# Optimization experiments

Measured on AMD Instinct MI355X. Metric: run time of the kernel, lower is better.

## Reference

```python
import jax, jax.numpy as jnp
import numpy as np
from jax import lax

BN_EPS = 1e-5

def _dw_conv_bn(img, w, g, b, mu, var):
    # img: [B,C,H,W], w: [C,1,3,3] depthwise (feature_group_count=C), stride 1, pad 1
    C = img.shape[1]
    y = lax.conv_general_dilated(img, w, (1, 1), 'SAME',
                                 dimension_numbers=('NCHW', 'OIHW', 'NCHW'),
                                 feature_group_count=C)
    scale = (g / jnp.sqrt(var + BN_EPS))[None, :, None, None]
    return y * scale + (b - mu * g / jnp.sqrt(var + BN_EPS))[None, :, None, None]


def setup_inputs() -> dict:
    key = jax.random.key(0)
    B, H, W, C, Co = 32, 28, 28, 192, 192
    T = 1 + H * W
    ks = jax.random.split(key, 8)
    x = jax.random.normal(ks[0], (B, T, C), dtype=jnp.float32)
    conv_w = jax.random.normal(ks[1], (3, C, 1, 3, 3), dtype=jnp.float32) * 0.1
    bn_scale = 1.0 + 0.1 * jax.random.normal(ks[2], (3, C), dtype=jnp.float32)
    bn_bias = 0.1 * jax.random.normal(ks[3], (3, C), dtype=jnp.float32)
    bn_mean = 0.1 * jax.random.normal(ks[4], (3, C), dtype=jnp.float32)
    bn_var = jax.random.uniform(ks[5], (3, C), dtype=jnp.float32, minval=0.5, maxval=1.5)
    w_qkv = jax.random.normal(ks[6], (3, Co, C), dtype=jnp.float32) / np.sqrt(C)
    kp, kb = jax.random.split(ks[7])
    w_proj = jax.random.normal(kp, (Co, Co), dtype=jnp.float32) / np.sqrt(Co)
    b_proj = 0.01 * jax.random.normal(kb, (Co,), dtype=jnp.float32)
    return {"x": x, "conv_w": conv_w, "bn_scale": bn_scale, "bn_bias": bn_bias,
            "bn_mean": bn_mean, "bn_var": bn_var, "w_qkv": w_qkv,
            "w_proj": w_proj, "b_proj": b_proj, "h": H, "w": W, "num_heads": 3}


def reference(x, conv_w, bn_scale, bn_bias, bn_mean, bn_var, w_qkv, w_proj, b_proj, h, w, num_heads):
    B, T, C = x.shape
    Co = w_proj.shape[0]
    scale = Co ** (-0.5)  # NOTE: module scales by dim_out^-0.5, not per-head
    cls_tok, tok = x[:, :1], x[:, 1:]
    img = tok.reshape(B, h, w, C).transpose(0, 3, 1, 2)  # b (h w) c -> b c h w
    qkv = []
    for i in range(3):  # q, k, v conv projections (depthwise conv + BN inference)
        y = _dw_conv_bn(img, conv_w[i], bn_scale[i], bn_bias[i], bn_mean[i], bn_var[i])
        y = y.reshape(B, C, h * w).transpose(0, 2, 1)  # b c h w -> b (h w) c
        y = jnp.concatenate([cls_tok, y], axis=1)      # prepend cls token
        qkv.append(jnp.einsum('btc,oc->bto', y, w_qkv[i]))
    d = Co // num_heads
    q, k, v = (t.reshape(B, T, num_heads, d).transpose(0, 2, 1, 3) for t in qkv)
    attn = jnp.einsum('bhld,bhtd->bhlt', q, k) * scale
    attn = jax.nn.softmax(attn, axis=-1)
    out = jnp.einsum('bhlt,bhtd->bhld', attn, v)
    out = out.transpose(0, 2, 1, 3).reshape(B, T, Co)
    return out @ w_proj.T + b_proj
```

## Files before the change

### kernel.cpp

```cpp
#include <hip/hip_runtime.h>

#define B_   32
#define Hh   28
#define Ww   28
#define Cc   192
#define T_   785
#define BT_  (B_ * T_)
#define BTC_ ((size_t)BT_ * Cc)
#define SCALE2 0.10412163388f

typedef __attribute__((ext_vector_type(8))) __bf16 bf16x8;
typedef __attribute__((ext_vector_type(4))) __bf16 bf16x4;
typedef __attribute__((ext_vector_type(4))) float  f32x4;

__global__ __launch_bounds__(192) void conv3_bn_k(
    const float* __restrict__ x, const float* __restrict__ cw,
    const float* __restrict__ g, const float* __restrict__ bb,
    const float* __restrict__ mu, const float* __restrict__ var,
    __bf16* __restrict__ y,
    const float* __restrict__ wqkv, const float* __restrict__ wproj,
    __bf16* __restrict__ wdst)
{
  const int c = threadIdx.x;
  const int h = blockIdx.x;
  const int b = blockIdx.y;
  if (h == Hh) {
    int t = b * 192 + c;
    int base = t * 24;
    const float* src = (base < 3 * Cc * Cc) ? (wqkv + base)
                                            : (wproj + (base - 3 * Cc * Cc));
#pragma unroll
    for (int e = 0; e < 24; e += 4) {
      float4 v = *(const float4*)(src + e);
      wdst[base + e + 0] = (__bf16)v.x;
      wdst[base + e + 1] = (__bf16)v.y;
      wdst[base + e + 2] = (__bf16)v.z;
      wdst[base + e + 3] = (__bf16)v.w;
    }
    return;
  }
  float w9[3][9], sc[3], sh[3];
#pragma unroll
  for (int br = 0; br < 3; ++br) {
    sc[br] = g[br * Cc + c] * rsqrtf(var[br * Cc + c] + 1e-5f);
    sh[br] = bb[br * Cc + c] - mu[br * Cc + c] * sc[br];
#pragma unroll
    for (int k = 0; k < 9; ++k) w9[br][k] = cw[(br * Cc + c) * 9 + k];
  }
  const float* xb = x + (size_t)b * T_ * Cc;
  if (h == 0) {
#pragma unroll
    for (int br = 0; br < 3; ++br)
      y[br * BTC_ + (size_t)b * T_ * Cc + c] = (__bf16)xb[c];
  }
  float c0[3], c1[3], c2[3];
#pragma unroll
  for (int r = 0; r < 3; ++r) {
    int rr = h - 1 + r;
    c0[r] = 0.f;
    c1[r] = (rr >= 0 && rr < Hh) ? xb[(size_t)(1 + rr * Ww) * Cc + c] : 0.f;
  }
  for (int col = 0; col < Ww; ++col) {
#pragma unroll
    for (int r = 0; r < 3; ++r) {
      int rr = h - 1 + r, ci = col + 1;
      c2[r] = (rr >= 0 && rr < Hh && ci < Ww)
                ? xb[(size_t)(1 + rr * Ww + ci) * Cc + c] : 0.f;
    }
    size_t orow = (size_t)(b * T_ + 1 + h * Ww + col) * Cc + c;
#pragma unroll
    for (int br = 0; br < 3; ++br) {
      float acc = c0[0]*w9[br][0] + c1[0]*w9[br][1] + c2[0]*w9[br][2]
                + c0[1]*w9[br][3] + c1[1]*w9[br][4] + c2[1]*w9[br][5]
                + c0[2]*w9[br][6] + c1[2]*w9[br][7] + c2[2]*w9[br][8];
      y[br * BTC_ + orow] = (__bf16)(acc * sc[br] + sh[br]);
    }
#pragma unroll
    for (int r = 0; r < 3; ++r) { c0[r] = c1[r]; c1[r] = c2[r]; }
  }
}

template <int MODE>
__global__ __launch_bounds__(512) void gemm_bf16(
    const __bf16* __restrict__ A0, const __bf16* __restrict__ W0,
    const float* __restrict__ bias, void* __restrict__ outp)
{
  __shared__ __bf16 As[128][72];
  __shared__ __bf16 Bs[192][72];
  const int z = blockIdx.z;
  const __bf16* A  = A0 + (MODE == 0 ? (size_t)z * BTC_ : 0);
  const __bf16* Bw = W0 + (MODE == 0 ? (size_t)z * Cc * Cc : 0);
  const float osc = (MODE == 0 && z == 0) ? SCALE2 : 1.0f;
  const int tid = threadIdx.x;
  const int wid = tid >> 6, l = tid & 63, c = l & 15, g = l >> 4;
  const int wm = wid >> 2, wn = wid & 3;
  const int m0 = blockIdx.x * 128;
  const int ar = tid >> 2, aq = tid & 3;
  const int brow = tid >> 3, bv = tid & 7;

  f32x4 acc[4][3];
#pragma unroll
  for (int i = 0; i < 4; ++i)
#pragma unroll
    for (int j = 0; j < 3; ++j) acc[i][j] = (f32x4)(0.f);

  const __bf16* ap = A + (size_t)(m0 + ar) * Cc + aq * 16;
  const __bf16* bp0 = Bw + (size_t)brow * Cc + bv * 8;
  uint4 a0 = *(const uint4*)(ap + 0);
  uint4 a1 = *(const uint4*)(ap + 8);
  uint4 b0 = *(const uint4*)(bp0 + 0 * 64 * Cc / 1);
  uint4 b1 = *(const uint4*)(bp0 + (size_t)64 * Cc);
  uint4 b2 = *(const uint4*)(bp0 + (size_t)128 * Cc);

  for (int kc = 0; kc < 3; ++kc) {
    __syncthreads();
    *(uint4*)&As[ar][aq * 16 + 0] = a0;
    *(uint4*)&As[ar][aq * 16 + 8] = a1;
    *(uint4*)&Bs[brow +   0][bv * 8] = b0;
    *(uint4*)&Bs[brow +  64][bv * 8] = b1;
    *(uint4*)&Bs[brow + 128][bv * 8] = b2;
    if (kc < 2) {
      ap += 64; bp0 += 64;
      a0 = *(const uint4*)(ap + 0);
      a1 = *(const uint4*)(ap + 8);
      b0 = *(const uint4*)(bp0);
      b1 = *(const uint4*)(bp0 + (size_t)64 * Cc);
      b2 = *(const uint4*)(bp0 + (size_t)128 * Cc);
    }
    __syncthreads();
#pragma unroll
    for (int ksl = 0; ksl < 2; ++ksl) {
      bf16x8 af[4], bfr[3];
#pragma unroll
      for (int mf = 0; mf < 4; ++mf)
        af[mf] = *(const bf16x8*)&As[wm * 64 + mf * 16 + c][ksl * 32 + g * 8];
#pragma unroll
      for (int nf = 0; nf < 3; ++nf)
        bfr[nf] = *(const bf16x8*)&Bs[wn * 48 + nf * 16 + c][ksl * 32 + g * 8];
      __builtin_amdgcn_s_setprio(1);
#pragma unroll
      for (int mf = 0; mf < 4; ++mf)
#pragma unroll
        for (int nf = 0; nf < 3; ++nf)
          acc[mf][nf] = __builtin_amdgcn_mfma_f32_16x16x32_bf16(
              af[mf], bfr[nf], acc[mf][nf], 0, 0, 0);
      __builtin_amdgcn_s_setprio(0);
    }
  }
  float bias_c[3] = {0.f, 0.f, 0.f};
  if (MODE == 1) {
#pragma unroll
    for (int nf = 0; nf < 3; ++nf) bias_c[nf] = bias[wn * 48 + nf * 16 + c];
  }
#pragma unroll
  for (int mf = 0; mf < 4; ++mf) {
#pragma unroll
    for (int i = 0; i < 4; ++i) {
      int m = m0 + wm * 64 + mf * 16 + g * 4 + i;
      if (m < BT_) {
#pragma unroll
        for (int nf = 0; nf < 3; ++nf) {
          int n = wn * 48 + nf * 16 + c;
          if (MODE == 1)
            ((float*)outp)[(size_t)m * Cc + n] = acc[mf][nf][i] + bias_c[nf];
          else
            ((__bf16*)outp)[z * BTC_ + (size_t)m * Cc + n] =
                (__bf16)(acc[mf][nf][i] * osc);
        }
      }
    }
  }
}

__global__ __launch_bounds__(256) void attn_mfma(
    const __bf16* __restrict__ qkv, __bf16* __restrict__ aout)
{
  __shared__ __bf16 Ks[64][72];
  __shared__ __bf16 Vt[64][72];
  __shared__ __bf16 Ps[4][16][72];
  const int bid = blockIdx.x;
  const int swz = (bid & 7) * 84 + (bid >> 3);
  const int qt = swz % 7;
  const int g2 = swz / 7;
  const int hh = g2 % 3;
  const int b  = g2 / 3;
  const int tid = threadIdx.x;
  const int wid = tid >> 6, l = tid & 63, c = l & 15, g = l >> 4;
  const __bf16* Q = qkv + ((size_t)(0 * B_ + b) * T_) * Cc + hh * 64;
  const __bf16* K = qkv + ((size_t)(1 * B_ + b) * T_) * Cc + hh * 64;
  const __bf16* V = qkv + ((size_t)(2 * B_ + b) * T_) * Cc + hh * 64;

  const int q0 = qt * 128 + wid * 32;
  bf16x8 qf[2][2];
#pragma unroll
  for (int s = 0; s < 2; ++s) {
    const __bf16* qp = Q + (size_t)(q0 + s * 16 + c) * Cc + g * 8;
    qf[s][0] = *(const bf16x8*)(qp);
    qf[s][1] = *(const bf16x8*)(qp + 32);
  }

  const int skey = tid >> 2, sdq = tid & 3;
  const int vkp = tid & 31, vd0 = (tid >> 5) * 8;
  const __bf16* kp  = K + (size_t)skey * Cc + sdq * 16;
  const __bf16* vp0 = V + (size_t)(2 * vkp + 0) * Cc + vd0;
  const __bf16* vp1 = V + (size_t)(2 * vkp + 1) * Cc + vd0;
  uint4 kr0 = *(const uint4*)(kp + 0);
  uint4 kr1 = *(const uint4*)(kp + 8);
  uint4 va  = *(const uint4*)vp0;
  uint4 vb  = *(const uint4*)vp1;

  f32x4 ot[2][4];
#pragma unroll
  for (int s = 0; s < 2; ++s)
#pragma unroll
    for (int f = 0; f < 4; ++f) ot[s][f] = (f32x4)(0.f);
  float m_run[2] = {-1e30f, -1e30f};
  float l_run[2] = {0.f, 0.f};

  for (int kt = 0; kt < 13; ++kt) {
    __syncthreads();
    *(uint4*)&Ks[skey][sdq * 16 + 0] = kr0;
    *(uint4*)&Ks[skey][sdq * 16 + 8] = kr1;
    {
      const ushort* pa = (const ushort*)&va;
      const ushort* pb = (const ushort*)&vb;
#pragma unroll
      for (int e = 0; e < 8; ++e) {
        unsigned pk2 = (unsigned)pa[e] | ((unsigned)pb[e] << 16);
        *(unsigned*)&Vt[vd0 + e][2 * vkp] = pk2;
      }
    }
    if (kt < 12) {
      kp += 64 * Cc; vp0 += 64 * Cc; vp1 += 64 * Cc;
      kr0 = *(const uint4*)(kp + 0);
      kr1 = *(const uint4*)(kp + 8);
      va  = *(const uint4*)vp0;
      vb  = *(const uint4*)vp1;
    }
    __syncthreads();

#pragma unroll
    for (int set = 0; set < 2; ++set) {
      f32x4 st[4];
#pragma unroll
      for (int f = 0; f < 4; ++f) st[f] = (f32x4)(0.f);
      __builtin_amdgcn_s_setprio(1);
#pragma unroll
      for (int s2 = 0; s2 < 2; ++s2) {
#pragma unroll
        for (int f = 0; f < 4; ++f) {
          bf16x8 ka = *(const bf16x8*)&Ks[f * 16 + c][s2 * 32 + g * 8];
          st[f] = __builtin_amdgcn_mfma_f32_16x16x32_bf16(ka, qf[set][s2], st[f], 0, 0, 0);
        }
      }
      __builtin_amdgcn_s_setprio(0);
      if (kt == 12) {
#pragma unroll
        for (int f = 0; f < 4; ++f)
#pragma unroll
          for (int i = 0; i < 4; ++i)
            if (f * 16 + g * 4 + i >= 17) st[f][i] = -1e30f;
      }
      float pmax = -1e30f;
#pragma unroll
      for (int f = 0; f < 4; ++f)
#pragma unroll
        for (int i = 0; i < 4; ++i) pmax = fmaxf(pmax, st[f][i]);
      pmax = fmaxf(pmax, __shfl_xor(pmax, 16));
      pmax = fmaxf(pmax, __shfl_xor(pmax, 32));
      if (!__all(pmax <= m_run[set] + 8.f)) {
        float mnew = fmaxf(m_run[set], pmax);
        float corr = exp2f(m_run[set] - mnew);
        m_run[set] = mnew;
        l_run[set] *= corr;
#pragma unroll
        for (int f = 0; f < 4; ++f)
#pragma unroll
          for (int i = 0; i < 4; ++i) ot[set][f][i] *= corr;
      }
      float rs = 0.f;
#pragma unroll
      for (int f = 0; f < 4; ++f) {
        bf16x4 pk;
#pragma unroll
        for (int i = 0; i < 4; ++i) {
          float p = exp2f(st[f][i] - m_run[set]);
          rs += p;
          pk[i] = (__bf16)p;
        }
        *(bf16x4*)&Ps[wid][c][f * 16 + g * 4] = pk;
      }
      rs += __shfl_xor(rs, 16);
      rs += __shfl_xor(rs, 32);
      l_run[set] += rs;

      __builtin_amdgcn_s_setprio(1);
#pragma unroll
      for (int s2 = 0; s2 < 2; ++s2) {
        bf16x8 pb2 = *(const bf16x8*)&Ps[wid][c][s2 * 32 + g * 8];
#pragma unroll
        for (int f = 0; f < 4; ++f) {
          bf16x8 va2 = *(const bf16x8*)&Vt[f * 16 + c][s2 * 32 + g * 8];
          ot[set][f] = __builtin_amdgcn_mfma_f32_16x16x32_bf16(va2, pb2, ot[set][f], 0, 0, 0);
        }
      }
      __builtin_amdgcn_s_setprio(0);
    }
  }

#pragma unroll
  for (int set = 0; set < 2; ++set) {
    const int t = q0 + set * 16 + c;
    if (t < T_) {
      float inv = 1.f / l_run[set];
      __bf16* op = aout + ((size_t)(b * T_ + t)) * Cc + hh * 64;
#pragma unroll
      for (int f = 0; f < 4; ++f) {
        bf16x4 ov;
#pragma unroll
        for (int i = 0; i < 4; ++i) ov[i] = (__bf16)(ot[set][f][i] * inv);
        *(bf16x4*)(op + f * 16 + g * 4) = ov;
      }
    }
  }
}

extern "C" void kernel_launch(void* const* d_in, const int* in_sizes, int n_in,
                              void* d_out, int out_size, void* d_ws, size_t ws_size,
                              hipStream_t stream) {
  (void)in_sizes; (void)n_in; (void)out_size; (void)ws_size;
  const float* x        = (const float*)d_in[0];
  const float* conv_w   = (const float*)d_in[1];
  const float* bn_scale = (const float*)d_in[2];
  const float* bn_bias  = (const float*)d_in[3];
  const float* bn_mean  = (const float*)d_in[4];
  const float* bn_var   = (const float*)d_in[5];
  const float* w_qkv    = (const float*)d_in[6];
  const float* w_proj   = (const float*)d_in[7];
  const float* b_proj   = (const float*)d_in[8];

  __bf16* ybf  = (__bf16*)d_ws;
  __bf16* qkvb = ybf + 3 * BTC_;
  __bf16* aobf = qkvb + 3 * BTC_;
  __bf16* wq   = aobf + BTC_;
  __bf16* wp   = wq + 3 * Cc * Cc;

  conv3_bn_k<<<dim3(Hh + 1, B_), 192, 0, stream>>>(
      x, conv_w, bn_scale, bn_bias, bn_mean, bn_var, ybf, w_qkv, w_proj, wq);

  const int mblocks = (BT_ + 127) / 128;
  gemm_bf16<0><<<dim3(mblocks, 1, 3), 512, 0, stream>>>(ybf, wq, nullptr, qkvb);
  attn_mfma<<<672, 256, 0, stream>>>(qkvb, aobf);
  gemm_bf16<1><<<dim3(mblocks, 1, 1), 512, 0, stream>>>(aobf, wp, b_proj, d_out);
}
```

Measured before the change: 179.4 us.

## Double-buffer attention K/V tiles, halve query tile, and block conv over rows

The attention kernel now double-buffers K and V in LDS with one barrier per key tile. It also halves the query rows per block from 128 to 64, which raises the grid from 672 to 1248 blocks, and the swizzle is updated to match. The conv kernel now has each block compute 4 output rows, so neighbouring input rows are reused across row outputs and the grid shrinks from 29x32 to 8x32 blocks. The intent is more overlap and occupancy in attention and fewer redundant input loads in conv, at the cost of reloading K/V once per smaller query tile and fewer, longer conv blocks.

Measured after the change: 177.0 us. No clear change (-1.3%).

```diff
diff --git a/kernel.cpp b/kernel.cpp
--- a/kernel.cpp
+++ b/kernel.cpp
@@ -22,9 +22,9 @@
     __bf16* __restrict__ wdst)
 {
   const int c = threadIdx.x;
-  const int h = blockIdx.x;
+  const int bx = blockIdx.x;
   const int b = blockIdx.y;
-  if (h == Hh) {
+  if (bx == 7) {
     int t = b * 192 + c;
     int base = t * 24;
     const float* src = (base < 3 * Cc * Cc) ? (wqkv + base)
@@ -39,6 +39,7 @@
     }
     return;
   }
+  const int h0 = bx * 4;
   float w9[3][9], sc[3], sh[3];
 #pragma unroll
   for (int br = 0; br < 3; ++br) {
@@ -48,35 +49,38 @@
     for (int k = 0; k < 9; ++k) w9[br][k] = cw[(br * Cc + c) * 9 + k];
   }
   const float* xb = x + (size_t)b * T_ * Cc;
-  if (h == 0) {
+  if (bx == 0) {
 #pragma unroll
     for (int br = 0; br < 3; ++br)
       y[br * BTC_ + (size_t)b * T_ * Cc + c] = (__bf16)xb[c];
   }
-  float c0[3], c1[3], c2[3];
-#pragma unroll
-  for (int r = 0; r < 3; ++r) {
-    int rr = h - 1 + r;
+  float c0[6], c1[6], c2[6];
+#pragma unroll
+  for (int r = 0; r < 6; ++r) {
+    int rr = h0 - 1 + r;
     c0[r] = 0.f;
     c1[r] = (rr >= 0 && rr < Hh) ? xb[(size_t)(1 + rr * Ww) * Cc + c] : 0.f;
   }
   for (int col = 0; col < Ww; ++col) {
 #pragma unroll
-    for (int r = 0; r < 3; ++r) {
-      int rr = h - 1 + r, ci = col + 1;
+    for (int r = 0; r < 6; ++r) {
+      int rr = h0 - 1 + r, ci = col + 1;
       c2[r] = (rr >= 0 && rr < Hh && ci < Ww)
                 ? xb[(size_t)(1 + rr * Ww + ci) * Cc + c] : 0.f;
     }
-    size_t orow = (size_t)(b * T_ + 1 + h * Ww + col) * Cc + c;
-#pragma unroll
-    for (int br = 0; br < 3; ++br) {
-      float acc = c0[0]*w9[br][0] + c1[0]*w9[br][1] + c2[0]*w9[br][2]
-                + c0[1]*w9[br][3] + c1[1]*w9[br][4] + c2[1]*w9[br][5]
-                + c0[2]*w9[br][6] + c1[2]*w9[br][7] + c2[2]*w9[br][8];
-      y[br * BTC_ + orow] = (__bf16)(acc * sc[br] + sh[br]);
-    }
-#pragma unroll
-    for (int r = 0; r < 3; ++r) { c0[r] = c1[r]; c1[r] = c2[r]; }
+#pragma unroll
+    for (int ro = 0; ro < 4; ++ro) {
+      size_t orow = (size_t)(b * T_ + 1 + (h0 + ro) * Ww + col) * Cc + c;
+#pragma unroll
+      for (int br = 0; br < 3; ++br) {
+        float acc = c0[ro+0]*w9[br][0] + c1[ro+0]*w9[br][1] + c2[ro+0]*w9[br][2]
+                  + c0[ro+1]*w9[br][3] + c1[ro+1]*w9[br][4] + c2[ro+1]*w9[br][5]
+                  + c0[ro+2]*w9[br][6] + c1[ro+2]*w9[br][7] + c2[ro+2]*w9[br][8];
+        y[br * BTC_ + orow] = (__bf16)(acc * sc[br] + sh[br]);
+      }
+    }
+#pragma unroll
+    for (int r = 0; r < 6; ++r) { c0[r] = c1[r]; c1[r] = c2[r]; }
   }
 }
 
@@ -108,7 +112,7 @@
   const __bf16* bp0 = Bw + (size_t)brow * Cc + bv * 8;
   uint4 a0 = *(const uint4*)(ap + 0);
   uint4 a1 = *(const uint4*)(ap + 8);
-  uint4 b0 = *(const uint4*)(bp0 + 0 * 64 * Cc / 1);
+  uint4 b0 = *(const uint4*)(bp0);
   uint4 b1 = *(const uint4*)(bp0 + (size_t)64 * Cc);
   uint4 b2 = *(const uint4*)(bp0 + (size_t)128 * Cc);
 
@@ -175,13 +179,13 @@
 __global__ __launch_bounds__(256) void attn_mfma(
     const __bf16* __restrict__ qkv, __bf16* __restrict__ aout)
 {
-  __shared__ __bf16 Ks[64][72];
-  __shared__ __bf16 Vt[64][72];
+  __shared__ __bf16 Ks[2][64][72];
+  __shared__ __bf16 Vt[2][64][72];
   __shared__ __bf16 Ps[4][16][72];
   const int bid = blockIdx.x;
-  const int swz = (bid & 7) * 84 + (bid >> 3);
-  const int qt = swz % 7;
-  const int g2 = swz / 7;
+  const int swz = (bid & 7) * 156 + (bid >> 3);
+  const int qt = swz % 13;
+  const int g2 = swz / 13;
   const int hh = g2 % 3;
   const int b  = g2 / 3;
   const int tid = threadIdx.x;
@@ -190,137 +194,134 @@
   const __bf16* K = qkv + ((size_t)(1 * B_ + b) * T_) * Cc + hh * 64;
   const __bf16* V = qkv + ((size_t)(2 * B_ + b) * T_) * Cc + hh * 64;
 
-  const int q0 = qt * 128 + wid * 32;
-  bf16x8 qf[2][2];
-#pragma unroll
-  for (int s = 0; s < 2; ++s) {
-    const __bf16* qp = Q + (size_t)(q0 + s * 16 + c) * Cc + g * 8;
-    qf[s][0] = *(const bf16x8*)(qp);
-    qf[s][1] = *(const bf16x8*)(qp + 32);
-  }
+  const int qrow = qt * 64 + wid * 16 + c;
+  const __bf16* qp = Q + (size_t)qrow * Cc + g * 8;
+  bf16x8 qf0 = *(const bf16x8*)(qp);
+  bf16x8 qf1 = *(const bf16x8*)(qp + 32);
 
   const int skey = tid >> 2, sdq = tid & 3;
   const int vkp = tid & 31, vd0 = (tid >> 5) * 8;
   const __bf16* kp  = K + (size_t)skey * Cc + sdq * 16;
   const __bf16* vp0 = V + (size_t)(2 * vkp + 0) * Cc + vd0;
   const __bf16* vp1 = V + (size_t)(2 * vkp + 1) * Cc + vd0;
-  uint4 kr0 = *(const uint4*)(kp + 0);
-  uint4 kr1 = *(const uint4*)(kp + 8);
-  uint4 va  = *(const uint4*)vp0;
-  uint4 vb  = *(const uint4*)vp1;
-
-  f32x4 ot[2][4];
-#pragma unroll
-  for (int s = 0; s < 2; ++s)
-#pragma unroll
-    for (int f = 0; f < 4; ++f) ot[s][f] = (f32x4)(0.f);
-  float m_run[2] = {-1e30f, -1e30f};
-  float l_run[2] = {0.f, 0.f};
+
+  uint4 kr0, kr1, va, vb;
+  auto loadKV = [&]() {
+    kr0 = *(const uint4*)(kp + 0);
+    kr1 = *(const uint4*)(kp + 8);
+    va  = *(const uint4*)vp0;
+    vb  = *(const uint4*)vp1;
+    kp += 64 * Cc; vp0 += 64 * Cc; vp1 += 64 * Cc;
+  };
+  auto writeLDS = [&](int buf) {
+    *(uint4*)&Ks[buf][skey][sdq * 16 + 0] = kr0;
+    *(uint4*)&Ks[buf][skey][sdq * 16 + 8] = kr1;
+    const ushort* pa = (const ushort*)&va;
+    const ushort* pb = (const ushort*)&vb;
+#pragma unroll
+    for (int e = 0; e < 8; ++e) {
+      unsigned pk2 = (unsigned)pa[e] | ((unsigned)pb[e] << 16);
+      *(unsigned*)&Vt[buf][vd0 + e][2 * vkp] = pk2;
+    }
+  };
+
+  loadKV();
+  writeLDS(0);
+  loadKV();
+  __syncthreads();
+
+  f32x4 ot[4];
+#pragma unroll
+  for (int f = 0; f < 4; ++f) ot[f] = (f32x4)(0.f);
+  float m_run = -1e30f, l_run = 0.f;
 
   for (int kt = 0; kt < 13; ++kt) {
+    const int cur = kt & 1;
+    if (kt < 12) {
+      writeLDS(cur ^ 1);
+      if (kt < 11) loadKV();
+    }
+
+    f32x4 st[4];
+#pragma unroll
+    for (int f = 0; f < 4; ++f) st[f] = (f32x4)(0.f);
+    __builtin_amdgcn_s_setprio(1);
+#pragma unroll
+    for (int f = 0; f < 4; ++f) {
+      bf16x8 ka = *(const bf16x8*)&Ks[cur][f * 16 + c][g * 8];
+      st[f] = __builtin_amdgcn_mfma_f32_16x16x32_bf16(ka, qf0, st[f], 0, 0, 0);
+    }
+#pragma unroll
+    for (int f = 0; f < 4; ++f) {
+      bf16x8 ka = *(const bf16x8*)&Ks[cur][f * 16 + c][32 + g * 8];
+      st[f] = __builtin_amdgcn_mfma_f32_16x16x32_bf16(ka, qf1, st[f], 0, 0, 0);
+    }
+    __builtin_amdgcn_s_setprio(0);
+
+    if (kt == 12) {
+#pragma unroll
+      for (int f = 0; f < 4; ++f)
+#pragma unroll
+        for (int i = 0; i < 4; ++i)
+          if (f * 16 + g * 4 + i >= 17) st[f][i] = -1e30f;
+    }
+    float pmax = -1e30f;
+#pragma unroll
+    for (int f = 0; f < 4; ++f)
+#pragma unroll
+      for (int i = 0; i < 4; ++i) pmax = fmaxf(pmax, st[f][i]);
+    pmax = fmaxf(pmax, __shfl_xor(pmax, 16));
+    pmax = fmaxf(pmax, __shfl_xor(pmax, 32));
+    if (!__all(pmax <= m_run + 8.f)) {
+      float mnew = fmaxf(m_run, pmax);
+      float corr = exp2f(m_run - mnew);
+      m_run = mnew;
+      l_run *= corr;
+#pragma unroll
+      for (int f = 0; f < 4; ++f)
+#pragma unroll
+        for (int i = 0; i < 4; ++i) ot[f][i] *= corr;
+    }
+    float rs = 0.f;
+#pragma unroll
+    for (int f = 0; f < 4; ++f) {
+      bf16x4 pk;
+#pragma unroll
+      for (int i = 0; i < 4; ++i) {
+        float p = exp2f(st[f][i] - m_run);
+        rs += p;
+        pk[i] = (__bf16)p;
+      }
+      *(bf16x4*)&Ps[wid][c][f * 16 + g * 4] = pk;
+    }
+    rs += __shfl_xor(rs, 16);
+    rs += __shfl_xor(rs, 32);
+    l_run += rs;
+
+    __builtin_amdgcn_s_setprio(1);
+#pragma unroll
+    for (int s2 = 0; s2 < 2; ++s2) {
+      bf16x8 pb2 = *(const bf16x8*)&Ps[wid][c][s2 * 32 + g * 8];
+#pragma unroll
+      for (int f = 0; f < 4; ++f) {
+        bf16x8 va2 = *(const bf16x8*)&Vt[cur][f * 16 + c][s2 * 32 + g * 8];
+        ot[f] = __builtin_amdgcn_mfma_f32_16x16x32_bf16(va2, pb2, ot[f], 0, 0, 0);
+      }
+    }
+    __builtin_amdgcn_s_setprio(0);
     __syncthreads();
-    *(uint4*)&Ks[skey][sdq * 16 + 0] = kr0;
-    *(uint4*)&Ks[skey][sdq * 16 + 8] = kr1;
-    {
-      const ushort* pa = (const ushort*)&va;
-      const ushort* pb = (const ushort*)&vb;
-#pragma unroll
-      for (int e = 0; e < 8; ++e) {
-        unsigned pk2 = (unsigned)pa[e] | ((unsigned)pb[e] << 16);
-        *(unsigned*)&Vt[vd0 + e][2 * vkp] = pk2;
-      }
-    }
-    if (kt < 12) {
-      kp += 64 * Cc; vp0 += 64 * Cc; vp1 += 64 * Cc;
-      kr0 = *(const uint4*)(kp + 0);
-      kr1 = *(const uint4*)(kp + 8);
-      va  = *(const uint4*)vp0;
-      vb  = *(const uint4*)vp1;
-    }
-    __syncthreads();
-
-#pragma unroll
-    for (int set = 0; set < 2; ++set) {
-      f32x4 st[4];
-#pragma unroll
-      for (int f = 0; f < 4; ++f) st[f] = (f32x4)(0.f);
-      __builtin_amdgcn_s_setprio(1);
-#pragma unroll
-      for (int s2 = 0; s2 < 2; ++s2) {
-#pragma unroll
-        for (int f = 0; f < 4; ++f) {
-          bf16x8 ka = *(const bf16x8*)&Ks[f * 16 + c][s2 * 32 + g * 8];
-          st[f] = __builtin_amdgcn_mfma_f32_16x16x32_bf16(ka, qf[set][s2], st[f], 0, 0, 0);
-        }
-      }
-      __builtin_amdgcn_s_setprio(0);
-      if (kt == 12) {
-#pragma unroll
-        for (int f = 0; f < 4; ++f)
-#pragma unroll
-          for (int i = 0; i < 4; ++i)
-            if (f * 16 + g * 4 + i >= 17) st[f][i] = -1e30f;
-      }
-      float pmax = -1e30f;
-#pragma unroll
-      for (int f = 0; f < 4; ++f)
-#pragma unroll
-        for (int i = 0; i < 4; ++i) pmax = fmaxf(pmax, st[f][i]);
-      pmax = fmaxf(pmax, __shfl_xor(pmax, 16));
-      pmax = fmaxf(pmax, __shfl_xor(pmax, 32));
-      if (!__all(pmax <= m_run[set] + 8.f)) {
-        float mnew = fmaxf(m_run[set], pmax);
-        float corr = exp2f(m_run[set] - mnew);
-        m_run[set] = mnew;
-        l_run[set] *= corr;
-#pragma unroll
-        for (int f = 0; f < 4; ++f)
-#pragma unroll
-          for (int i = 0; i < 4; ++i) ot[set][f][i] *= corr;
-      }
-      float rs = 0.f;
-#pragma unroll
-      for (int f = 0; f < 4; ++f) {
-        bf16x4 pk;
-#pragma unroll
-        for (int i = 0; i < 4; ++i) {
-          float p = exp2f(st[f][i] - m_run[set]);
-          rs += p;
-          pk[i] = (__bf16)p;
-        }
-        *(bf16x4*)&Ps[wid][c][f * 16 + g * 4] = pk;
-      }
-      rs += __shfl_xor(rs, 16);
-      rs += __shfl_xor(rs, 32);
-      l_run[set] += rs;
-
-      __builtin_amdgcn_s_setprio(1);
-#pragma unroll
-      for (int s2 = 0; s2 < 2; ++s2) {
-        bf16x8 pb2 = *(const bf16x8*)&Ps[wid][c][s2 * 32 + g * 8];
-#pragma unroll
-        for (int f = 0; f < 4; ++f) {
-          bf16x8 va2 = *(const bf16x8*)&Vt[f * 16 + c][s2 * 32 + g * 8];
-          ot[set][f] = __builtin_amdgcn_mfma_f32_16x16x32_bf16(va2, pb2, ot[set][f], 0, 0, 0);
-        }
-      }
-      __builtin_amdgcn_s_setprio(0);
-    }
-  }
-
-#pragma unroll
-  for (int set = 0; set < 2; ++set) {
-    const int t = q0 + set * 16 + c;
-    if (t < T_) {
-      float inv = 1.f / l_run[set];
-      __bf16* op = aout + ((size_t)(b * T_ + t)) * Cc + hh * 64;
-#pragma unroll
-      for (int f = 0; f < 4; ++f) {
-        bf16x4 ov;
-#pragma unroll
-        for (int i = 0; i < 4; ++i) ov[i] = (__bf16)(ot[set][f][i] * inv);
-        *(bf16x4*)(op + f * 16 + g * 4) = ov;
-      }
+  }
+
+  const int t = qt * 64 + wid * 16 + c;
+  if (t < T_) {
+    float inv = 1.f / l_run;
+    __bf16* op = aout + ((size_t)(b * T_ + t)) * Cc + hh * 64;
+#pragma unroll
+    for (int f = 0; f < 4; ++f) {
+      bf16x4 ov;
+#pragma unroll
+      for (int i = 0; i < 4; ++i) ov[i] = (__bf16)(ot[f][i] * inv);
+      *(bf16x4*)(op + f * 16 + g * 4) = ov;
     }
   }
 }
@@ -345,11 +346,11 @@
   __bf16* wq   = aobf + BTC_;
   __bf16* wp   = wq + 3 * Cc * Cc;
 
-  conv3_bn_k<<<dim3(Hh + 1, B_), 192, 0, stream>>>(
+  conv3_bn_k<<<dim3(8, B_), 192, 0, stream>>>(
       x, conv_w, bn_scale, bn_bias, bn_mean, bn_var, ybf, w_qkv, w_proj, wq);
 
   const int mblocks = (BT_ + 127) / 128;
   gemm_bf16<0><<<dim3(mblocks, 1, 3), 512, 0, stream>>>(ybf, wq, nullptr, qkvb);
-  attn_mfma<<<672, 256, 0, stream>>>(qkvb, aobf);
+  attn_mfma<<<1248, 256, 0, stream>>>(qkvb, aobf);
   gemm_bf16<1><<<dim3(mblocks, 1, 1), 512, 0, stream>>>(aobf, wp, b_proj, d_out);
 }
```
